# Kernel optimization log

Hardware: AMD Instinct MI355X
Metric: run time of the kernel (lower is better)

## Reference

```python
import jax, jax.numpy as jnp
import numpy as np

E, HEADS, HD, L, FF = 768, 12, 64, 12, 3072


def layernorm(x, g, b, eps=1e-5):
    m = jnp.mean(x, axis=-1, keepdims=True)
    v = jnp.var(x, axis=-1, keepdims=True)
    return (x - m) / jnp.sqrt(v + eps) * g + b


def setup_inputs() -> dict:
    key = jax.random.key(0)
    ks = jax.random.split(key, 26)
    B, N, PS = 32, 1024, 24
    P2 = PS * PS
    def rn(k, shape, s=0.02):
        return jax.random.normal(k, shape, dtype=jnp.float32) * s
    return {
        "scene_masks": jax.random.normal(ks[0], (B, N, PS, PS), dtype=jnp.float32),
        "target_mask": jax.random.normal(ks[1], (B, PS, PS), dtype=jnp.float32),
        "emb_W": rn(ks[2], (E, P2)),            # torch Linear weight [out,in]
        "emb_b": rn(ks[3], (E,)),
        "class_embed": rn(ks[4], (1, 1, E)),
        "scene_pos": rn(ks[5], (1, N + 1, E)),
        "target_pos": rn(ks[6], (1, 2, E)),
        "ln1_g": jnp.ones((L, E), jnp.float32),
        "ln1_b": jnp.zeros((L, E), jnp.float32),
        "ln2_g": jnp.ones((L, E), jnp.float32),
        "ln2_b": jnp.zeros((L, E), jnp.float32),
        "Wq": rn(ks[7], (L, HD, HD)),
        "Wk": rn(ks[8], (L, HD, HD)),
        "Wv": rn(ks[9], (L, HD, HD)),
        "Wo": rn(ks[10], (L, E, E)),
        "bo": rn(ks[11], (L, E)),
        "W1": rn(ks[12], (L, FF, E)),
        "b1": rn(ks[13], (L, FF)),
        "W2": rn(ks[14], (L, E, FF)),
        "b2": rn(ks[15], (L, E)),
        "mlp_W": rn(ks[16], (N, E)),
        "mlp_b": rn(ks[17], (N,)),
    }


def _forward_logits(scene_masks, target_mask, emb_W, emb_b, class_embed, scene_pos,
                    target_pos, ln1_g, ln1_b, ln2_g, ln2_b, Wq, Wk, Wv, Wo, bo,
                    W1, b1, W2, b2, mlp_W, mlp_b):
    B, N, H, W = scene_masks.shape
    P2 = H * W
    scene = scene_masks.reshape(B, N, P2) @ emb_W.T + emb_b          # [B,N,E]
    tgt = target_mask.reshape(B, 1, P2) @ emb_W.T + emb_b            # [B,1,E]
    cls = jnp.broadcast_to(class_embed, (B, 1, E))
    scene = jnp.concatenate([cls, scene], axis=1) + scene_pos[:, :N + 1]  # [B,N+1,E]
    tgt = jnp.concatenate([cls, tgt], axis=1) + target_pos               # [B,2,E]
    scale = jnp.sqrt(jnp.float32(E))

    def block(tq, p):
        g1, bb1n, g2, bb2n, wq, wk, wv, wo, bo_, w1, b1_, w2, b2_ = p
        kv = layernorm(scene, g1, bb1n)                # norm1(value)=norm1(key)
        q = layernorm(tq, g1, bb1n)                    # norm1(query)
        kvh = kv.reshape(B, N + 1, HEADS, HD)
        qh = q.reshape(B, 2, HEADS, HD)
        # per-head Linear shares one [HD,HD] weight across all heads
        qs = jnp.einsum('nqhd,ed->nqhe', qh, wq)
        ks_ = jnp.einsum('nkhd,ed->nkhe', kvh, wk)
        vs = jnp.einsum('nkhd,ed->nkhe', kvh, wv)
        energy = jnp.einsum('nqhd,nkhd->nhqk', qs, ks_)     # [B,H,2,N+1]
        att = jax.nn.softmax(energy / scale, axis=-1)
        out = jnp.einsum('nhqk,nkhd->nqhd', att, vs).reshape(B, 2, E)
        out = out @ wo.T + bo_
        x = layernorm(out + tq, g1, bb1n)
        ff = jax.nn.relu(x @ w1.T + b1_) @ w2.T + b2_
        return layernorm(ff + x, g2, bb2n), None

    params = (ln1_g, ln1_b, ln2_g, ln2_b, Wq, Wk, Wv, Wo, bo, W1, b1, W2, b2)
    tgt, _ = jax.lax.scan(block, tgt, params)
    x = jnp.mean(tgt, axis=1) @ mlp_W.T + mlp_b       # [B, num_patches]
    return x


def reference(scene_masks, target_mask, emb_W, emb_b, class_embed, scene_pos,
              target_pos, ln1_g, ln1_b, ln2_g, ln2_b, Wq, Wk, Wv, Wo, bo,
              W1, b1, W2, b2, mlp_W, mlp_b):
    x = _forward_logits(scene_masks, target_mask, emb_W, emb_b, class_embed,
                        scene_pos, target_pos, ln1_g, ln1_b, ln2_g, ln2_b,
                        Wq, Wk, Wv, Wo, bo, W1, b1, W2, b2, mlp_W, mlp_b)
    # sorted_nodes = argsort desc + 1; eye(P+1)[nodes-1] == one_hot(argsort desc)
    order = jnp.argsort(-x, axis=1)[:, :5]                # top-5 patch indices
    return jax.nn.one_hot(order, x.shape[1] + 1, dtype=jnp.float32)  # [B,5,P+1]
```

## Files before the change

### kernel.cpp

```cpp
#include <hip/hip_runtime.h>
#include <math.h>

#define E_DIM 768
#define NTOK 1025
#define B_DIM 32
#define NHEADS 12
#define HDIM 64
#define LAYERS 12
#define FF_DIM 3072
#define P2 576

__device__ __forceinline__ float block_reduce_sum(float v, float* red) {
  int tid = threadIdx.x;
  red[tid] = v;
  __syncthreads();
#pragma unroll
  for (int s = 128; s > 0; s >>= 1) {
    if (tid < s) red[tid] += red[tid + s];
    __syncthreads();
  }
  float r = red[0];
  __syncthreads();
  return r;
}

__global__ __launch_bounds__(256) void embed_gemm(
    const float* __restrict__ A, const float* __restrict__ W,
    const float* __restrict__ bias, const float* __restrict__ pos,
    float* __restrict__ scene) {
  __shared__ float Xs[16][132];
  __shared__ float Ws[16][132];
  int tid = threadIdx.x;
  int n0 = blockIdx.x * 128;
  int m0 = blockIdx.y * 128;
  int lr = tid >> 2;
  int lk = (tid & 3) << 2;
  int ty = tid >> 4, tx = tid & 15;
  float acc[8][8] = {};
  for (int k0 = 0; k0 < P2; k0 += 16) {
    float4 x0 = *(const float4*)(A + (size_t)(m0 + lr) * P2 + k0 + lk);
    float4 x1 = *(const float4*)(A + (size_t)(m0 + 64 + lr) * P2 + k0 + lk);
    float4 w0 = *(const float4*)(W + (size_t)(n0 + lr) * P2 + k0 + lk);
    float4 w1 = *(const float4*)(W + (size_t)(n0 + 64 + lr) * P2 + k0 + lk);
    __syncthreads();
    Xs[lk + 0][lr] = x0.x; Xs[lk + 1][lr] = x0.y; Xs[lk + 2][lr] = x0.z; Xs[lk + 3][lr] = x0.w;
    Xs[lk + 0][64 + lr] = x1.x; Xs[lk + 1][64 + lr] = x1.y; Xs[lk + 2][64 + lr] = x1.z; Xs[lk + 3][64 + lr] = x1.w;
    Ws[lk + 0][lr] = w0.x; Ws[lk + 1][lr] = w0.y; Ws[lk + 2][lr] = w0.z; Ws[lk + 3][lr] = w0.w;
    Ws[lk + 0][64 + lr] = w1.x; Ws[lk + 1][64 + lr] = w1.y; Ws[lk + 2][64 + lr] = w1.z; Ws[lk + 3][64 + lr] = w1.w;
    __syncthreads();
#pragma unroll
    for (int kk = 0; kk < 16; ++kk) {
      float4 a0 = *(const float4*)&Xs[kk][ty << 2];
      float4 a1 = *(const float4*)&Xs[kk][64 + (ty << 2)];
      float4 b0 = *(const float4*)&Ws[kk][tx << 2];
      float4 b1 = *(const float4*)&Ws[kk][64 + (tx << 2)];
      float av[8] = {a0.x, a0.y, a0.z, a0.w, a1.x, a1.y, a1.z, a1.w};
      float bv[8] = {b0.x, b0.y, b0.z, b0.w, b1.x, b1.y, b1.z, b1.w};
#pragma unroll
      for (int i = 0; i < 8; ++i)
#pragma unroll
        for (int j = 0; j < 8; ++j) acc[i][j] += av[i] * bv[j];
    }
  }
#pragma unroll
  for (int i = 0; i < 8; ++i) {
    int mloc = (i < 4) ? ((ty << 2) + i) : (64 + (ty << 2) + i - 4);
    int m = m0 + mloc;
    int b = m >> 10, nt = m & 1023;
    size_t row = ((size_t)b * NTOK + 1 + nt) * E_DIM;
    size_t prow = (size_t)(1 + nt) * E_DIM;
#pragma unroll
    for (int half = 0; half < 2; ++half) {
      int n = n0 + half * 64 + (tx << 2);
      float4 o4;
      o4.x = acc[i][half * 4 + 0] + bias[n + 0] + pos[prow + n + 0];
      o4.y = acc[i][half * 4 + 1] + bias[n + 1] + pos[prow + n + 1];
      o4.z = acc[i][half * 4 + 2] + bias[n + 2] + pos[prow + n + 2];
      o4.w = acc[i][half * 4 + 3] + bias[n + 3] + pos[prow + n + 3];
      *(float4*)&scene[row + n] = o4;
    }
  }
}

__global__ void scene_cls(const float* __restrict__ cls, const float* __restrict__ pos,
                          float* __restrict__ scene) {
  int b = blockIdx.x;
  for (int e = threadIdx.x; e < E_DIM; e += 256)
    scene[(size_t)b * NTOK * E_DIM + e] = cls[e] + pos[e];
}

__global__ __launch_bounds__(256) void ln_rows(const float* __restrict__ in, float* __restrict__ out) {
  __shared__ float red[256];
  int r = blockIdx.x, tid = threadIdx.x;
  const float* x = in + (size_t)r * E_DIM;
  float a0 = x[tid], a1 = x[tid + 256], a2 = x[tid + 512];
  float mean = block_reduce_sum(a0 + a1 + a2, red) * (1.f / 768.f);
  float d0 = a0 - mean, d1 = a1 - mean, d2 = a2 - mean;
  float var = block_reduce_sum(d0 * d0 + d1 * d1 + d2 * d2, red) * (1.f / 768.f);
  float rinv = rsqrtf(var + 1e-5f);
  float* o = out + (size_t)r * E_DIM;
  o[tid] = d0 * rinv; o[tid + 256] = d1 * rinv; o[tid + 512] = d2 * rinv;
}

__global__ __launch_bounds__(256) void tgt_init(
    const float* __restrict__ tmask, const float* __restrict__ W,
    const float* __restrict__ bias, const float* __restrict__ cls,
    const float* __restrict__ tpos, float* __restrict__ tq) {
  int b = blockIdx.x, tid = threadIdx.x;
  for (int e = tid; e < E_DIM; e += 256)
    tq[(size_t)(b * 2) * E_DIM + e] = cls[e] + tpos[e];
  const float* tm = tmask + (size_t)b * P2;
  for (int e = tid; e < E_DIM; e += 256) {
    const float* wr = W + (size_t)e * P2;
    float s = 0.f;
    for (int k = 0; k < P2; k += 4) {
      float4 w4 = *(const float4*)&wr[k];
      float4 t4 = *(const float4*)&tm[k];
      s += w4.x * t4.x + w4.y * t4.y + w4.z * t4.z + w4.w * t4.w;
    }
    tq[(size_t)(b * 2 + 1) * E_DIM + e] = s + bias[e] + tpos[E_DIM + e];
  }
}

__global__ void prep_m(const float* __restrict__ Wq, const float* __restrict__ Wk,
                       float* __restrict__ Mb) {
  int l = blockIdx.y;
  int idx = blockIdx.x * 256 + threadIdx.x;
  int d = idx >> 6, dp = idx & 63;
  const float* wq = Wq + l * 4096;
  const float* wk = Wk + l * 4096;
  float s = 0.f;
#pragma unroll 8
  for (int e = 0; e < 64; ++e) s += wq[e * 64 + d] * wk[e * 64 + dp];
  Mb[l * 4096 + idx] = s;
}

__global__ void prep_wvo(const float* __restrict__ Wv, const float* __restrict__ Wo,
                         float* __restrict__ Wvo) {
  int l = blockIdx.y;
  int idx = blockIdx.x * 256 + threadIdx.x;
  int ep = idx / 768, hd = idx % 768;
  int h = hd >> 6, d = hd & 63;
  const float* wv = Wv + (size_t)l * 4096;
  const float* wo = Wo + (size_t)l * 768 * 768 + (size_t)ep * 768 + h * 64;
  float s = 0.f;
#pragma unroll 8
  for (int ev = 0; ev < 64; ++ev) s += wv[ev * 64 + d] * wo[ev];
  Wvo[(size_t)l * 589824 + idx] = s;
}

__global__ __launch_bounds__(256) void qln_qm(
    const float* __restrict__ tq, const float* __restrict__ g1,
    const float* __restrict__ b1, const float* __restrict__ Mb, int l,
    float* __restrict__ qMg, float* __restrict__ qMb) {
  __shared__ float q[768];
  __shared__ float qm[768];
  __shared__ float red[256];
  int r = blockIdx.x, tid = threadIdx.x;
  const float* x = tq + (size_t)r * E_DIM;
  float a0 = x[tid], a1 = x[tid + 256], a2 = x[tid + 512];
  float mean = block_reduce_sum(a0 + a1 + a2, red) * (1.f / 768.f);
  float d0 = a0 - mean, d1 = a1 - mean, d2 = a2 - mean;
  float var = block_reduce_sum(d0 * d0 + d1 * d1 + d2 * d2, red) * (1.f / 768.f);
  float rinv = rsqrtf(var + 1e-5f);
  const float* gl = g1 + l * E_DIM;
  const float* bl = b1 + l * E_DIM;
  q[tid] = d0 * rinv * gl[tid] + bl[tid];
  q[tid + 256] = d1 * rinv * gl[tid + 256] + bl[tid + 256];
  q[tid + 512] = d2 * rinv * gl[tid + 512] + bl[tid + 512];
  __syncthreads();
  const float* M = Mb + l * 4096;
  const float inv_scale = rsqrtf(768.f);
  for (int o = tid; o < 768; o += 256) {
    int h = o >> 6, dp = o & 63;
    const float* qh = q + h * 64;
    float s = 0.f;
#pragma unroll 8
    for (int d = 0; d < 64; ++d) s += qh[d] * M[d * 64 + dp];
    qm[o] = s;
    qMg[(size_t)r * E_DIM + o] = s * gl[o] * inv_scale;
  }
  __syncthreads();
  if (tid < NHEADS) {
    float acc = 0.f;
#pragma unroll 8
    for (int dp = 0; dp < 64; ++dp) acc += qm[tid * 64 + dp] * bl[tid * 64 + dp];
    qMb[r * NHEADS + tid] = acc * inv_scale;
  }
}

#define ACH 272
__global__ __launch_bounds__(256) void attn_flash(
    const float* __restrict__ ns, const float* __restrict__ qMg,
    const float* __restrict__ qMb, const float* __restrict__ g1,
    const float* __restrict__ b1, int l, float* __restrict__ ctx) {
  __shared__ float red[256];
  __shared__ float sred[2][16];
  __shared__ float cred[2][16][64];
  int b = blockIdx.x / NHEADS;
  int h = blockIdx.x % NHEADS;
  int tid = threadIdx.x;
  int g = tid >> 4;
  int lane = tid & 15;
  int r0 = b * 2, r1 = r0 + 1;
  const float* nsb = ns + (size_t)b * NTOK * E_DIM + h * 64;
  float4 q0v = *(const float4*)(qMg + (size_t)r0 * E_DIM + h * 64 + lane * 4);
  float4 q1v = *(const float4*)(qMg + (size_t)r1 * E_DIM + h * 64 + lane * 4);
  float qb0 = qMb[r0 * NHEADS + h], qb1 = qMb[r1 * NHEADS + h];
  float m = -1e30f, s0 = 0.f, s1 = 0.f;
  float4 c0 = {0, 0, 0, 0}, c1 = {0, 0, 0, 0};
  float4 v[17];
  float e0a[17], e1a[17];
  for (int cb = 0; cb < NTOK; cb += ACH) {
    int ntk = NTOK - cb; if (ntk > ACH) ntk = ACH;
    int cnt = (ntk - g + 15) >> 4;
    float mloc = -1e30f;
#pragma unroll
    for (int i = 0; i < 17; ++i) {
      if (i < cnt) {
        int k = cb + g + (i << 4);
        float4 vv = *(const float4*)(nsb + (size_t)k * E_DIM + lane * 4);
        v[i] = vv;
        float p0 = vv.x * q0v.x + vv.y * q0v.y + vv.z * q0v.z + vv.w * q0v.w;
        float p1 = vv.x * q1v.x + vv.y * q1v.y + vv.z * q1v.z + vv.w * q1v.w;
#pragma unroll
        for (int off = 8; off; off >>= 1) {
          p0 += __shfl_xor(p0, off, 16);
          p1 += __shfl_xor(p1, off, 16);
        }
        float e0 = p0 + qb0, e1 = p1 + qb1;
        e0a[i] = e0; e1a[i] = e1;
        mloc = fmaxf(mloc, fmaxf(e0, e1));
      }
    }
    red[tid] = mloc;
    __syncthreads();
#pragma unroll
    for (int s = 128; s > 0; s >>= 1) {
      if (tid < s) red[tid] = fmaxf(red[tid], red[tid + s]);
      __syncthreads();
    }
    float mnew = fmaxf(m, red[0]);
    __syncthreads();
    if (mnew > m) {
      float f = expf(m - mnew);
      s0 *= f; s1 *= f;
      c0.x *= f; c0.y *= f; c0.z *= f; c0.w *= f;
      c1.x *= f; c1.y *= f; c1.z *= f; c1.w *= f;
      m = mnew;
    }
#pragma unroll
    for (int i = 0; i < 17; ++i) {
      if (i < cnt) {
        float p0 = expf(e0a[i] - m);
        float p1 = expf(e1a[i] - m);
        s0 += p0; s1 += p1;
        c0.x += p0 * v[i].x; c0.y += p0 * v[i].y; c0.z += p0 * v[i].z; c0.w += p0 * v[i].w;
        c1.x += p1 * v[i].x; c1.y += p1 * v[i].y; c1.z += p1 * v[i].z; c1.w += p1 * v[i].w;
      }
    }
  }
  if (lane == 0) { sred[0][g] = s0; sred[1][g] = s1; }
  *(float4*)&cred[0][g][lane * 4] = c0;
  *(float4*)&cred[1][g][lane * 4] = c1;
  __syncthreads();
  if (tid < 128) {
    int t = tid >> 6, dd = tid & 63;
    int o = h * 64 + dd;
    float stot = 0.f, cs = 0.f;
#pragma unroll
    for (int gg = 0; gg < 16; ++gg) { stot += sred[t][gg]; cs += cred[t][gg][dd]; }
    float inv = 1.f / stot;
    ctx[(size_t)(r0 + t) * E_DIM + o] = cs * inv * g1[l * E_DIM + o] + b1[l * E_DIM + o];
  }
}

__global__ __launch_bounds__(256) void skinny_part(
    const float* __restrict__ X, int K, const float* __restrict__ W,
    int kchunk, float* __restrict__ part, int N) {
  __shared__ float Xs[16][64];
  __shared__ float Ws[16][64];
  int tid = threadIdx.x;
  int n0 = blockIdx.x * 64;
  int s = blockIdx.y;
  int kbeg = s * kchunk;
  int lr = tid >> 2;
  int lk = (tid & 3) << 2;
  int ty = tid >> 4, tx = tid & 15;
  float acc[4][4] = {};
  for (int k0 = kbeg; k0 < kbeg + kchunk; k0 += 16) {
    float4 xv = *(const float4*)(X + (size_t)lr * K + k0 + lk);
    float4 wv = *(const float4*)(W + (size_t)(n0 + lr) * K + k0 + lk);
    __syncthreads();
    Xs[lk + 0][lr] = xv.x; Xs[lk + 1][lr] = xv.y; Xs[lk + 2][lr] = xv.z; Xs[lk + 3][lr] = xv.w;
    Ws[lk + 0][lr] = wv.x; Ws[lk + 1][lr] = wv.y; Ws[lk + 2][lr] = wv.z; Ws[lk + 3][lr] = wv.w;
    __syncthreads();
#pragma unroll
    for (int kk = 0; kk < 16; ++kk) {
      float4 a4 = *(const float4*)&Xs[kk][ty << 2];
      float4 b4 = *(const float4*)&Ws[kk][tx << 2];
      float av[4] = {a4.x, a4.y, a4.z, a4.w};
      float bv[4] = {b4.x, b4.y, b4.z, b4.w};
#pragma unroll
      for (int i = 0; i < 4; ++i)
#pragma unroll
        for (int j = 0; j < 4; ++j) acc[i][j] += av[i] * bv[j];
    }
  }
#pragma unroll
  for (int i = 0; i < 4; ++i) {
    int mm = (ty << 2) + i;
    float4 o4 = make_float4(acc[i][0], acc[i][1], acc[i][2], acc[i][3]);
    *(float4*)&part[((size_t)s * 64 + mm) * N + n0 + (tx << 2)] = o4;
  }
}

__global__ __launch_bounds__(256) void skinny_h1_part(
    const float* __restrict__ part1, const float* __restrict__ b1,
    const float* __restrict__ W, int kchunk, float* __restrict__ part2) {
  __shared__ float Xs[16][64];
  __shared__ float Ws[16][64];
  const int K = 3072, N = 768;
  int tid = threadIdx.x;
  int n0 = blockIdx.x * 64;
  int s = blockIdx.y;
  int kbeg = s * kchunk;
  int lr = tid >> 2;
  int lk = (tid & 3) << 2;
  int ty = tid >> 4, tx = tid & 15;
  float acc[4][4] = {};
  for (int k0 = kbeg; k0 < kbeg + kchunk; k0 += 16) {
    float4 x0 = *(const float4*)(part1 + (size_t)lr * K + k0 + lk);
    float4 x1 = *(const float4*)(part1 + (size_t)(64 + lr) * K + k0 + lk);
    float4 x2 = *(const float4*)(part1 + (size_t)(128 + lr) * K + k0 + lk);
    float4 x3 = *(const float4*)(part1 + (size_t)(192 + lr) * K + k0 + lk);
    float4 bb = *(const float4*)(b1 + k0 + lk);
    float4 xv;
    xv.x = fmaxf(x0.x + x1.x + x2.x + x3.x + bb.x, 0.f);
    xv.y = fmaxf(x0.y + x1.y + x2.y + x3.y + bb.y, 0.f);
    xv.z = fmaxf(x0.z + x1.z + x2.z + x3.z + bb.z, 0.f);
    xv.w = fmaxf(x0.w + x1.w + x2.w + x3.w + bb.w, 0.f);
    float4 wv = *(const float4*)(W + (size_t)(n0 + lr) * K + k0 + lk);
    __syncthreads();
    Xs[lk + 0][lr] = xv.x; Xs[lk + 1][lr] = xv.y; Xs[lk + 2][lr] = xv.z; Xs[lk + 3][lr] = xv.w;
    Ws[lk + 0][lr] = wv.x; Ws[lk + 1][lr] = wv.y; Ws[lk + 2][lr] = wv.z; Ws[lk + 3][lr] = wv.w;
    __syncthreads();
#pragma unroll
    for (int kk = 0; kk < 16; ++kk) {
      float4 a4 = *(const float4*)&Xs[kk][ty << 2];
      float4 b4 = *(const float4*)&Ws[kk][tx << 2];
      float av[4] = {a4.x, a4.y, a4.z, a4.w};
      float bv[4] = {b4.x, b4.y, b4.z, b4.w};
#pragma unroll
      for (int i = 0; i < 4; ++i)
#pragma unroll
        for (int j = 0; j < 4; ++j) acc[i][j] += av[i] * bv[j];
    }
  }
#pragma unroll
  for (int i = 0; i < 4; ++i) {
    int mm = (ty << 2) + i;
    float4 o4 = make_float4(acc[i][0], acc[i][1], acc[i][2], acc[i][3]);
    *(float4*)&part2[((size_t)s * 64 + mm) * N + n0 + (tx << 2)] = o4;
  }
}

__global__ __launch_bounds__(256) void reduce_ln_q(
    const float* __restrict__ part, int S, const float* __restrict__ bias,
    const float* __restrict__ res, const float* __restrict__ g,
    const float* __restrict__ bsh, float* __restrict__ out,
    const float* __restrict__ Mb_next, const float* __restrict__ g1n,
    const float* __restrict__ b1n, float* __restrict__ qMg,
    float* __restrict__ qMb, float* __restrict__ xmean) {
  __shared__ float red[256];
  __shared__ float q[768];
  __shared__ float qm[768];
  int m = blockIdx.x, tid = threadIdx.x;
  float t[3];
#pragma unroll
  for (int c = 0; c < 3; ++c) {
    int n = tid + c * 256;
    float s = 0.f;
    for (int i = 0; i < S; ++i) s += part[((size_t)i * 64 + m) * 768 + n];
    t[c] = s + bias[n] + res[(size_t)m * 768 + n];
  }
  float mean = block_reduce_sum(t[0] + t[1] + t[2], red) * (1.f / 768.f);
  float d0 = t[0] - mean, d1 = t[1] - mean, d2 = t[2] - mean;
  float var = block_reduce_sum(d0 * d0 + d1 * d1 + d2 * d2, red) * (1.f / 768.f);
  float rinv = rsqrtf(var + 1e-5f);
  float y0 = d0 * rinv * g[tid] + bsh[tid];
  float y1 = d1 * rinv * g[tid + 256] + bsh[tid + 256];
  float y2 = d2 * rinv * g[tid + 512] + bsh[tid + 512];
  out[(size_t)m * 768 + tid] = y0;
  out[(size_t)m * 768 + tid + 256] = y1;
  out[(size_t)m * 768 + tid + 512] = y2;
  if (xmean) {
    float* xr = xmean + (size_t)(m >> 1) * 768;
    atomicAdd(&xr[tid], 0.5f * y0);
    atomicAdd(&xr[tid + 256], 0.5f * y1);
    atomicAdd(&xr[tid + 512], 0.5f * y2);
  }
  if (Mb_next) {
    float mean2 = block_reduce_sum(y0 + y1 + y2, red) * (1.f / 768.f);
    float e0 = y0 - mean2, e1 = y1 - mean2, e2 = y2 - mean2;
    float var2 = block_reduce_sum(e0 * e0 + e1 * e1 + e2 * e2, red) * (1.f / 768.f);
    float rinv2 = rsqrtf(var2 + 1e-5f);
    q[tid] = e0 * rinv2 * g1n[tid] + b1n[tid];
    q[tid + 256] = e1 * rinv2 * g1n[tid + 256] + b1n[tid + 256];
    q[tid + 512] = e2 * rinv2 * g1n[tid + 512] + b1n[tid + 512];
    __syncthreads();
    const float inv_scale = rsqrtf(768.f);
    for (int o = tid; o < 768; o += 256) {
      int h = o >> 6, dp = o & 63;
      const float* qh = q + h * 64;
      float s = 0.f;
#pragma unroll 8
      for (int d = 0; d < 64; ++d) s += qh[d] * Mb_next[d * 64 + dp];
      qm[o] = s;
      qMg[(size_t)m * E_DIM + o] = s * g1n[o] * inv_scale;
    }
    __syncthreads();
    if (tid < NHEADS) {
      float acc = 0.f;
#pragma unroll 8
      for (int dp = 0; dp < 64; ++dp) acc += qm[tid * 64 + dp] * b1n[tid * 64 + dp];
      qMb[m * NHEADS + tid] = acc * inv_scale;
    }
  }
}

__global__ __launch_bounds__(256) void top5_from_parts(
    const float* __restrict__ part, const float* __restrict__ bias,
    float* __restrict__ out) {
  __shared__ float v[1024];
  __shared__ float bv[256];
  __shared__ int bi[256];
  int b = blockIdx.x, tid = threadIdx.x;
  for (int i = tid; i < 1024; i += 256) {
    float s = part[(size_t)(0 * 64 + b) * 1024 + i] + part[(size_t)(1 * 64 + b) * 1024 + i] +
              part[(size_t)(2 * 64 + b) * 1024 + i] + part[(size_t)(3 * 64 + b) * 1024 + i];
    v[i] = s + bias[i];
  }
  float* ob = out + (size_t)b * 5 * NTOK;
  for (int i = tid; i < 5 * NTOK; i += 256) ob[i] = 0.f;
  __syncthreads();
  for (int it = 0; it < 5; ++it) {
    float best = -1e38f;
    int bidx = 0x7fffffff;
    for (int i = tid; i < 1024; i += 256) {
      float x = v[i];
      if (x > best || (x == best && i < bidx)) { best = x; bidx = i; }
    }
    bv[tid] = best; bi[tid] = bidx;
    __syncthreads();
    for (int s = 128; s > 0; s >>= 1) {
      if (tid < s) {
        if (bv[tid + s] > bv[tid] || (bv[tid + s] == bv[tid] && bi[tid + s] < bi[tid])) {
          bv[tid] = bv[tid + s]; bi[tid] = bi[tid + s];
        }
      }
      __syncthreads();
    }
    if (tid == 0) {
      ob[it * NTOK + bi[0]] = 1.0f;
      v[bi[0]] = -1e38f;
    }
    __syncthreads();
  }
}

extern "C" void kernel_launch(void* const* d_in, const int* in_sizes, int n_in,
                              void* d_out, int out_size, void* d_ws, size_t ws_size,
                              hipStream_t stream) {
  const float* scene_masks = (const float*)d_in[0];
  const float* target_mask = (const float*)d_in[1];
  const float* emb_W = (const float*)d_in[2];
  const float* emb_b = (const float*)d_in[3];
  const float* class_embed = (const float*)d_in[4];
  const float* scene_pos = (const float*)d_in[5];
  const float* target_pos = (const float*)d_in[6];
  const float* ln1_g = (const float*)d_in[7];
  const float* ln1_b = (const float*)d_in[8];
  const float* ln2_g = (const float*)d_in[9];
  const float* ln2_b = (const float*)d_in[10];
  const float* Wq = (const float*)d_in[11];
  const float* Wk = (const float*)d_in[12];
  const float* Wv = (const float*)d_in[13];
  const float* Wo = (const float*)d_in[14];
  const float* bo = (const float*)d_in[15];
  const float* W1 = (const float*)d_in[16];
  const float* fb1 = (const float*)d_in[17];
  const float* W2 = (const float*)d_in[18];
  const float* fb2 = (const float*)d_in[19];
  const float* mlp_W = (const float*)d_in[20];
  const float* mlp_b = (const float*)d_in[21];
  float* out = (float*)d_out;

  float* ws = (float*)d_ws;
  float* scene = ws;
  float* Mbuf = scene + 25190400;
  float* Wvo = Mbuf + 49152;
  float* tq = Wvo + 7077888;
  float* qMg = tq + 49152;
  float* qMb = qMg + 49152;
  float* ctxf = qMb + 768;
  float* xbuf = ctxf + 49152;
  float* xm = xbuf + 49152;
  float* partA = xm + 49152;
  float* partB = partA + 786432;

  embed_gemm<<<dim3(6, 256), 256, 0, stream>>>(scene_masks, emb_W, emb_b, scene_pos, scene);
  scene_cls<<<32, 256, 0, stream>>>(class_embed, scene_pos, scene);
  ln_rows<<<32 * NTOK, 256, 0, stream>>>(scene, scene);
  tgt_init<<<32, 256, 0, stream>>>(target_mask, emb_W, emb_b, class_embed, target_pos, tq);
  prep_m<<<dim3(16, 12), 256, 0, stream>>>(Wq, Wk, Mbuf);
  prep_wvo<<<dim3(2304, 12), 256, 0, stream>>>(Wv, Wo, Wvo);
  hipMemsetAsync(xm, 0, 49152 * sizeof(float), stream);
  qln_qm<<<64, 256, 0, stream>>>(tq, ln1_g, ln1_b, Mbuf, 0, qMg, qMb);

  for (int l = 0; l < LAYERS; ++l) {
    attn_flash<<<32 * NHEADS, 256, 0, stream>>>(scene, qMg, qMb, ln1_g, ln1_b, l, ctxf);
    skinny_part<<<dim3(12, 8), 256, 0, stream>>>(ctxf, 768, Wvo + (size_t)l * 589824, 96, partA, 768);
    reduce_ln_q<<<64, 256, 0, stream>>>(partA, 8, bo + l * 768, tq,
                                        ln1_g + l * 768, ln1_b + l * 768, xbuf,
                                        nullptr, nullptr, nullptr, nullptr, nullptr, nullptr);
    skinny_part<<<dim3(48, 4), 256, 0, stream>>>(xbuf, 768, W1 + (size_t)l * FF_DIM * 768, 192, partB, FF_DIM);
    skinny_h1_part<<<dim3(12, 16), 256, 0, stream>>>(partB, fb1 + l * FF_DIM,
                                                     W2 + (size_t)l * 768 * FF_DIM, 192, partA);
    if (l < LAYERS - 1)
      reduce_ln_q<<<64, 256, 0, stream>>>(partA, 16, fb2 + l * 768, xbuf,
                                          ln2_g + l * 768, ln2_b + l * 768, tq,
                                          Mbuf + (l + 1) * 4096, ln1_g + (l + 1) * 768,
                                          ln1_b + (l + 1) * 768, qMg, qMb, nullptr);
    else
      reduce_ln_q<<<64, 256, 0, stream>>>(partA, 16, fb2 + l * 768, xbuf,
                                          ln2_g + l * 768, ln2_b + l * 768, tq,
                                          nullptr, nullptr, nullptr, nullptr, nullptr, xm);
  }

  skinny_part<<<dim3(16, 4), 256, 0, stream>>>(xm, 768, mlp_W, 192, partA, 1024);
  top5_from_parts<<<32, 256, 0, stream>>>(partA, mlp_b, out);
}
```

Baseline: 1.929 ms.

## Fuse query LN/projection into attention and restructure per-layer MLP kernels

Each attention block now recomputes the query layernorm and its M-projection for its own head, so the separate q kernel and the q work inside reduce_ln go away. A new projln kernel fuses the Wvo projection, bias, residual and layernorm, replacing a split-K GEMM plus a reduce pass. The FF1 GEMM now runs without a K split and applies bias and ReLU in its epilogue, and the FF2 split count drops from 16 to 4. This cuts launches and partial-sum traffic but lowers parallelism: projln runs only 16 blocks and FF1 only 48, and each attention block redundantly recomputes the layernorm.

```diff
diff --git a/kernel.cpp b/kernel.cpp
--- a/kernel.cpp
+++ b/kernel.cpp
@@ -149,64 +149,62 @@
   Wvo[(size_t)l * 589824 + idx] = s;
 }
 
-__global__ __launch_bounds__(256) void qln_qm(
-    const float* __restrict__ tq, const float* __restrict__ g1,
-    const float* __restrict__ b1, const float* __restrict__ Mb, int l,
-    float* __restrict__ qMg, float* __restrict__ qMb) {
-  __shared__ float q[768];
-  __shared__ float qm[768];
+#define ACH 272
+__global__ __launch_bounds__(256) void attn_flash_q(
+    const float* __restrict__ tq, const float* __restrict__ Mb,
+    const float* __restrict__ g1, const float* __restrict__ b1, int l,
+    const float* __restrict__ ns, float* __restrict__ ctx) {
   __shared__ float red[256];
-  int r = blockIdx.x, tid = threadIdx.x;
-  const float* x = tq + (size_t)r * E_DIM;
-  float a0 = x[tid], a1 = x[tid + 256], a2 = x[tid + 512];
-  float mean = block_reduce_sum(a0 + a1 + a2, red) * (1.f / 768.f);
-  float d0 = a0 - mean, d1 = a1 - mean, d2 = a2 - mean;
-  float var = block_reduce_sum(d0 * d0 + d1 * d1 + d2 * d2, red) * (1.f / 768.f);
-  float rinv = rsqrtf(var + 1e-5f);
-  const float* gl = g1 + l * E_DIM;
-  const float* bl = b1 + l * E_DIM;
-  q[tid] = d0 * rinv * gl[tid] + bl[tid];
-  q[tid + 256] = d1 * rinv * gl[tid + 256] + bl[tid + 256];
-  q[tid + 512] = d2 * rinv * gl[tid + 512] + bl[tid + 512];
-  __syncthreads();
-  const float* M = Mb + l * 4096;
-  const float inv_scale = rsqrtf(768.f);
-  for (int o = tid; o < 768; o += 256) {
-    int h = o >> 6, dp = o & 63;
-    const float* qh = q + h * 64;
-    float s = 0.f;
-#pragma unroll 8
-    for (int d = 0; d < 64; ++d) s += qh[d] * M[d * 64 + dp];
-    qm[o] = s;
-    qMg[(size_t)r * E_DIM + o] = s * gl[o] * inv_scale;
-  }
-  __syncthreads();
-  if (tid < NHEADS) {
-    float acc = 0.f;
-#pragma unroll 8
-    for (int dp = 0; dp < 64; ++dp) acc += qm[tid * 64 + dp] * bl[tid * 64 + dp];
-    qMb[r * NHEADS + tid] = acc * inv_scale;
-  }
-}
-
-#define ACH 272
-__global__ __launch_bounds__(256) void attn_flash(
-    const float* __restrict__ ns, const float* __restrict__ qMg,
-    const float* __restrict__ qMb, const float* __restrict__ g1,
-    const float* __restrict__ b1, int l, float* __restrict__ ctx) {
-  __shared__ float red[256];
+  __shared__ float qs[2][64];
+  __shared__ float qg[2][64];
+  __shared__ float qmb[2];
   __shared__ float sred[2][16];
   __shared__ float cred[2][16][64];
   int b = blockIdx.x / NHEADS;
   int h = blockIdx.x % NHEADS;
   int tid = threadIdx.x;
+  const float* gl = g1 + l * E_DIM;
+  const float* bl = b1 + l * E_DIM;
+  int seg = h >> 2;
+  int base = h * 64 - seg * 256;
+  for (int r = 0; r < 2; ++r) {
+    const float* x = tq + (size_t)(b * 2 + r) * E_DIM;
+    float a0 = x[tid], a1 = x[tid + 256], a2 = x[tid + 512];
+    float mean = block_reduce_sum(a0 + a1 + a2, red) * (1.f / 768.f);
+    float d0 = a0 - mean, d1 = a1 - mean, d2 = a2 - mean;
+    float var = block_reduce_sum(d0 * d0 + d1 * d1 + d2 * d2, red) * (1.f / 768.f);
+    float rinv = rsqrtf(var + 1e-5f);
+    float dv = (seg == 0) ? d0 : ((seg == 1) ? d1 : d2);
+    if (tid >= base && tid < base + 64) {
+      int d = tid - base;
+      qs[r][d] = dv * rinv * gl[h * 64 + d] + bl[h * 64 + d];
+    }
+  }
+  __syncthreads();
+  const float inv_scale = rsqrtf(768.f);
+  if (tid < 128) {
+    int r = tid >> 6, dp = tid & 63;
+    const float* M = Mb + l * 4096;
+    float s = 0.f;
+#pragma unroll 8
+    for (int d = 0; d < 64; ++d) s += qs[r][d] * M[d * 64 + dp];
+    qg[r][dp] = s * gl[h * 64 + dp] * inv_scale;
+    red[tid] = s * bl[h * 64 + dp];
+  }
+  __syncthreads();
+  if (tid < 2) {
+    float a = 0.f;
+    for (int dp = 0; dp < 64; ++dp) a += red[tid * 64 + dp];
+    qmb[tid] = a * inv_scale;
+  }
+  __syncthreads();
   int g = tid >> 4;
   int lane = tid & 15;
   int r0 = b * 2, r1 = r0 + 1;
   const float* nsb = ns + (size_t)b * NTOK * E_DIM + h * 64;
-  float4 q0v = *(const float4*)(qMg + (size_t)r0 * E_DIM + h * 64 + lane * 4);
-  float4 q1v = *(const float4*)(qMg + (size_t)r1 * E_DIM + h * 64 + lane * 4);
-  float qb0 = qMb[r0 * NHEADS + h], qb1 = qMb[r1 * NHEADS + h];
+  float4 q0v = *(const float4*)&qg[0][lane * 4];
+  float4 q1v = *(const float4*)&qg[1][lane * 4];
+  float qb0 = qmb[0], qb1 = qmb[1];
   float m = -1e30f, s0 = 0.f, s1 = 0.f;
   float4 c0 = {0, 0, 0, 0}, c1 = {0, 0, 0, 0};
   float4 v[17];
@@ -271,13 +269,69 @@
 #pragma unroll
     for (int gg = 0; gg < 16; ++gg) { stot += sred[t][gg]; cs += cred[t][gg][dd]; }
     float inv = 1.f / stot;
-    ctx[(size_t)(r0 + t) * E_DIM + o] = cs * inv * g1[l * E_DIM + o] + b1[l * E_DIM + o];
+    ctx[(size_t)(r0 + t) * E_DIM + o] = cs * inv * gl[o] + bl[o];
+  }
+}
+
+__global__ __launch_bounds__(256) void projln(
+    const float* __restrict__ ctx, const float* __restrict__ Wvo_l,
+    const float* __restrict__ bo_l, const float* __restrict__ tq,
+    const float* __restrict__ gl, const float* __restrict__ bl,
+    float* __restrict__ x) {
+  __shared__ float cx[4][768];
+  __shared__ float pr[4][768];
+  __shared__ float red[256];
+  int r0 = blockIdx.x * 4;
+  int tid = threadIdx.x;
+  int g = tid >> 4, lane = tid & 15;
+  for (int i = tid; i < 4 * 768; i += 256) {
+    int rr = i / 768, cc = i % 768;
+    cx[rr][cc] = ctx[(size_t)(r0 + rr) * 768 + cc];
+  }
+  __syncthreads();
+  for (int n = g; n < 768; n += 16) {
+    const float* w = Wvo_l + (size_t)n * 768;
+    float a0 = 0.f, a1 = 0.f, a2 = 0.f, a3 = 0.f;
+    for (int k = lane * 4; k < 768; k += 64) {
+      float4 wv = *(const float4*)(w + k);
+      float4 v0 = *(const float4*)&cx[0][k];
+      float4 v1 = *(const float4*)&cx[1][k];
+      float4 v2 = *(const float4*)&cx[2][k];
+      float4 v3 = *(const float4*)&cx[3][k];
+      a0 += wv.x * v0.x + wv.y * v0.y + wv.z * v0.z + wv.w * v0.w;
+      a1 += wv.x * v1.x + wv.y * v1.y + wv.z * v1.z + wv.w * v1.w;
+      a2 += wv.x * v2.x + wv.y * v2.y + wv.z * v2.z + wv.w * v2.w;
+      a3 += wv.x * v3.x + wv.y * v3.y + wv.z * v3.z + wv.w * v3.w;
+    }
+#pragma unroll
+    for (int off = 8; off; off >>= 1) {
+      a0 += __shfl_xor(a0, off, 16);
+      a1 += __shfl_xor(a1, off, 16);
+      a2 += __shfl_xor(a2, off, 16);
+      a3 += __shfl_xor(a3, off, 16);
+    }
+    if (lane == 0) { pr[0][n] = a0; pr[1][n] = a1; pr[2][n] = a2; pr[3][n] = a3; }
+  }
+  __syncthreads();
+  for (int r = 0; r < 4; ++r) {
+    int row = r0 + r;
+    float t0 = pr[r][tid] + bo_l[tid] + tq[(size_t)row * 768 + tid];
+    float t1 = pr[r][tid + 256] + bo_l[tid + 256] + tq[(size_t)row * 768 + tid + 256];
+    float t2 = pr[r][tid + 512] + bo_l[tid + 512] + tq[(size_t)row * 768 + tid + 512];
+    float mean = block_reduce_sum(t0 + t1 + t2, red) * (1.f / 768.f);
+    float d0 = t0 - mean, d1 = t1 - mean, d2 = t2 - mean;
+    float var = block_reduce_sum(d0 * d0 + d1 * d1 + d2 * d2, red) * (1.f / 768.f);
+    float rinv = rsqrtf(var + 1e-5f);
+    x[(size_t)row * 768 + tid] = d0 * rinv * gl[tid] + bl[tid];
+    x[(size_t)row * 768 + tid + 256] = d1 * rinv * gl[tid + 256] + bl[tid + 256];
+    x[(size_t)row * 768 + tid + 512] = d2 * rinv * gl[tid + 512] + bl[tid + 512];
   }
 }
 
 __global__ __launch_bounds__(256) void skinny_part(
     const float* __restrict__ X, int K, const float* __restrict__ W,
-    int kchunk, float* __restrict__ part, int N) {
+    int kchunk, float* __restrict__ part, int N,
+    const float* __restrict__ bias, int relu) {
   __shared__ float Xs[16][64];
   __shared__ float Ws[16][64];
   int tid = threadIdx.x;
@@ -311,70 +365,24 @@
   for (int i = 0; i < 4; ++i) {
     int mm = (ty << 2) + i;
     float4 o4 = make_float4(acc[i][0], acc[i][1], acc[i][2], acc[i][3]);
+    if (bias) {
+      int n = n0 + (tx << 2);
+      o4.x += bias[n + 0]; o4.y += bias[n + 1]; o4.z += bias[n + 2]; o4.w += bias[n + 3];
+      if (relu) {
+        o4.x = fmaxf(o4.x, 0.f); o4.y = fmaxf(o4.y, 0.f);
+        o4.z = fmaxf(o4.z, 0.f); o4.w = fmaxf(o4.w, 0.f);
+      }
+    }
     *(float4*)&part[((size_t)s * 64 + mm) * N + n0 + (tx << 2)] = o4;
   }
 }
 
-__global__ __launch_bounds__(256) void skinny_h1_part(
-    const float* __restrict__ part1, const float* __restrict__ b1,
-    const float* __restrict__ W, int kchunk, float* __restrict__ part2) {
-  __shared__ float Xs[16][64];
-  __shared__ float Ws[16][64];
-  const int K = 3072, N = 768;
-  int tid = threadIdx.x;
-  int n0 = blockIdx.x * 64;
-  int s = blockIdx.y;
-  int kbeg = s * kchunk;
-  int lr = tid >> 2;
-  int lk = (tid & 3) << 2;
-  int ty = tid >> 4, tx = tid & 15;
-  float acc[4][4] = {};
-  for (int k0 = kbeg; k0 < kbeg + kchunk; k0 += 16) {
-    float4 x0 = *(const float4*)(part1 + (size_t)lr * K + k0 + lk);
-    float4 x1 = *(const float4*)(part1 + (size_t)(64 + lr) * K + k0 + lk);
-    float4 x2 = *(const float4*)(part1 + (size_t)(128 + lr) * K + k0 + lk);
-    float4 x3 = *(const float4*)(part1 + (size_t)(192 + lr) * K + k0 + lk);
-    float4 bb = *(const float4*)(b1 + k0 + lk);
-    float4 xv;
-    xv.x = fmaxf(x0.x + x1.x + x2.x + x3.x + bb.x, 0.f);
-    xv.y = fmaxf(x0.y + x1.y + x2.y + x3.y + bb.y, 0.f);
-    xv.z = fmaxf(x0.z + x1.z + x2.z + x3.z + bb.z, 0.f);
-    xv.w = fmaxf(x0.w + x1.w + x2.w + x3.w + bb.w, 0.f);
-    float4 wv = *(const float4*)(W + (size_t)(n0 + lr) * K + k0 + lk);
-    __syncthreads();
-    Xs[lk + 0][lr] = xv.x; Xs[lk + 1][lr] = xv.y; Xs[lk + 2][lr] = xv.z; Xs[lk + 3][lr] = xv.w;
-    Ws[lk + 0][lr] = wv.x; Ws[lk + 1][lr] = wv.y; Ws[lk + 2][lr] = wv.z; Ws[lk + 3][lr] = wv.w;
-    __syncthreads();
-#pragma unroll
-    for (int kk = 0; kk < 16; ++kk) {
-      float4 a4 = *(const float4*)&Xs[kk][ty << 2];
-      float4 b4 = *(const float4*)&Ws[kk][tx << 2];
-      float av[4] = {a4.x, a4.y, a4.z, a4.w};
-      float bv[4] = {b4.x, b4.y, b4.z, b4.w};
-#pragma unroll
-      for (int i = 0; i < 4; ++i)
-#pragma unroll
-        for (int j = 0; j < 4; ++j) acc[i][j] += av[i] * bv[j];
-    }
-  }
-#pragma unroll
-  for (int i = 0; i < 4; ++i) {
-    int mm = (ty << 2) + i;
-    float4 o4 = make_float4(acc[i][0], acc[i][1], acc[i][2], acc[i][3]);
-    *(float4*)&part2[((size_t)s * 64 + mm) * N + n0 + (tx << 2)] = o4;
-  }
-}
-
-__global__ __launch_bounds__(256) void reduce_ln_q(
+__global__ __launch_bounds__(256) void reduce_ln(
     const float* __restrict__ part, int S, const float* __restrict__ bias,
     const float* __restrict__ res, const float* __restrict__ g,
     const float* __restrict__ bsh, float* __restrict__ out,
-    const float* __restrict__ Mb_next, const float* __restrict__ g1n,
-    const float* __restrict__ b1n, float* __restrict__ qMg,
-    float* __restrict__ qMb, float* __restrict__ xmean) {
+    float* __restrict__ xmean) {
   __shared__ float red[256];
-  __shared__ float q[768];
-  __shared__ float qm[768];
   int m = blockIdx.x, tid = threadIdx.x;
   float t[3];
 #pragma unroll
@@ -399,33 +407,6 @@
     atomicAdd(&xr[tid], 0.5f * y0);
     atomicAdd(&xr[tid + 256], 0.5f * y1);
     atomicAdd(&xr[tid + 512], 0.5f * y2);
-  }
-  if (Mb_next) {
-    float mean2 = block_reduce_sum(y0 + y1 + y2, red) * (1.f / 768.f);
-    float e0 = y0 - mean2, e1 = y1 - mean2, e2 = y2 - mean2;
-    float var2 = block_reduce_sum(e0 * e0 + e1 * e1 + e2 * e2, red) * (1.f / 768.f);
-    float rinv2 = rsqrtf(var2 + 1e-5f);
-    q[tid] = e0 * rinv2 * g1n[tid] + b1n[tid];
-    q[tid + 256] = e1 * rinv2 * g1n[tid + 256] + b1n[tid + 256];
-    q[tid + 512] = e2 * rinv2 * g1n[tid + 512] + b1n[tid + 512];
-    __syncthreads();
-    const float inv_scale = rsqrtf(768.f);
-    for (int o = tid; o < 768; o += 256) {
-      int h = o >> 6, dp = o & 63;
-      const float* qh = q + h * 64;
-      float s = 0.f;
-#pragma unroll 8
-      for (int d = 0; d < 64; ++d) s += qh[d] * Mb_next[d * 64 + dp];
-      qm[o] = s;
-      qMg[(size_t)m * E_DIM + o] = s * g1n[o] * inv_scale;
-    }
-    __syncthreads();
-    if (tid < NHEADS) {
-      float acc = 0.f;
-#pragma unroll 8
-      for (int dp = 0; dp < 64; ++dp) acc += qm[tid * 64 + dp] * b1n[tid * 64 + dp];
-      qMb[m * NHEADS + tid] = acc * inv_scale;
-    }
   }
 }
 
@@ -501,13 +482,11 @@
   float* Mbuf = scene + 25190400;
   float* Wvo = Mbuf + 49152;
   float* tq = Wvo + 7077888;
-  float* qMg = tq + 49152;
-  float* qMb = qMg + 49152;
-  float* ctxf = qMb + 768;
+  float* ctxf = tq + 49152;
   float* xbuf = ctxf + 49152;
-  float* xm = xbuf + 49152;
+  float* h1 = xbuf + 49152;
+  float* xm = h1 + 196608;
   float* partA = xm + 49152;
-  float* partB = partA + 786432;
 
   embed_gemm<<<dim3(6, 256), 256, 0, stream>>>(scene_masks, emb_W, emb_b, scene_pos, scene);
   scene_cls<<<32, 256, 0, stream>>>(class_embed, scene_pos, scene);
@@ -516,28 +495,20 @@
   prep_m<<<dim3(16, 12), 256, 0, stream>>>(Wq, Wk, Mbuf);
   prep_wvo<<<dim3(2304, 12), 256, 0, stream>>>(Wv, Wo, Wvo);
   hipMemsetAsync(xm, 0, 49152 * sizeof(float), stream);
-  qln_qm<<<64, 256, 0, stream>>>(tq, ln1_g, ln1_b, Mbuf, 0, qMg, qMb);
 
   for (int l = 0; l < LAYERS; ++l) {
-    attn_flash<<<32 * NHEADS, 256, 0, stream>>>(scene, qMg, qMb, ln1_g, ln1_b, l, ctxf);
-    skinny_part<<<dim3(12, 8), 256, 0, stream>>>(ctxf, 768, Wvo + (size_t)l * 589824, 96, partA, 768);
-    reduce_ln_q<<<64, 256, 0, stream>>>(partA, 8, bo + l * 768, tq,
-                                        ln1_g + l * 768, ln1_b + l * 768, xbuf,
-                                        nullptr, nullptr, nullptr, nullptr, nullptr, nullptr);
-    skinny_part<<<dim3(48, 4), 256, 0, stream>>>(xbuf, 768, W1 + (size_t)l * FF_DIM * 768, 192, partB, FF_DIM);
-    skinny_h1_part<<<dim3(12, 16), 256, 0, stream>>>(partB, fb1 + l * FF_DIM,
-                                                     W2 + (size_t)l * 768 * FF_DIM, 192, partA);
-    if (l < LAYERS - 1)
-      reduce_ln_q<<<64, 256, 0, stream>>>(partA, 16, fb2 + l * 768, xbuf,
-                                          ln2_g + l * 768, ln2_b + l * 768, tq,
-                                          Mbuf + (l + 1) * 4096, ln1_g + (l + 1) * 768,
-                                          ln1_b + (l + 1) * 768, qMg, qMb, nullptr);
-    else
-      reduce_ln_q<<<64, 256, 0, stream>>>(partA, 16, fb2 + l * 768, xbuf,
-                                          ln2_g + l * 768, ln2_b + l * 768, tq,
-                                          nullptr, nullptr, nullptr, nullptr, nullptr, xm);
-  }
-
-  skinny_part<<<dim3(16, 4), 256, 0, stream>>>(xm, 768, mlp_W, 192, partA, 1024);
+    attn_flash_q<<<32 * NHEADS, 256, 0, stream>>>(tq, Mbuf, ln1_g, ln1_b, l, scene, ctxf);
+    projln<<<16, 256, 0, stream>>>(ctxf, Wvo + (size_t)l * 589824, bo + l * 768,
+                                   tq, ln1_g + l * 768, ln1_b + l * 768, xbuf);
+    skinny_part<<<dim3(48, 1), 256, 0, stream>>>(xbuf, 768, W1 + (size_t)l * FF_DIM * 768,
+                                                 768, h1, FF_DIM, fb1 + l * FF_DIM, 1);
+    skinny_part<<<dim3(12, 4), 256, 0, stream>>>(h1, FF_DIM, W2 + (size_t)l * 768 * FF_DIM,
+                                                 768, partA, 768, nullptr, 0);
+    reduce_ln<<<64, 256, 0, stream>>>(partA, 4, fb2 + l * 768, xbuf,
+                                      ln2_g + l * 768, ln2_b + l * 768, tq,
+                                      (l == LAYERS - 1) ? xm : nullptr);
+  }
+
+  skinny_part<<<dim3(16, 4), 256, 0, stream>>>(xm, 768, mlp_W, 192, partA, 1024, nullptr, 0);
   top5_from_parts<<<32, 256, 0, stream>>>(partA, mlp_b, out);
 }
```

New measurement: 5.116 ms. 2.65x slower.
